# Kernel optimization log

Measured on AMD Instinct MI355X. Metric: run time of the kernel, lower is better.

The kernel has to match this reference:

```python
import jax, jax.numpy as jnp
import numpy as np

G = 8          # grid_size
DH = 32        # dim_head
EPS = 1e-5
INIT_LS = 1e-5


def setup_inputs() -> dict:
    key = jax.random.key(0)
    ks = jax.random.split(key, 8)
    B, H, W, C = 16, 128, 128, 256
    s = 1.0 / np.sqrt(C)
    return {
        "x": jax.random.normal(ks[0], (B, H, W, C), dtype=jnp.float32),
        "ln_w": jnp.ones((C,), jnp.float32),
        "ln_b": jnp.zeros((C,), jnp.float32),
        "in_proj_w": jax.random.uniform(ks[1], (3 * C, C), jnp.float32, -s, s),
        "in_proj_b": jnp.zeros((3 * C,), jnp.float32),
        "out_proj_w": jax.random.uniform(ks[2], (C, C), jnp.float32, -s, s),
        "out_proj_b": jnp.zeros((C,), jnp.float32),
        "gamma": jnp.full((C,), INIT_LS, jnp.float32),
    }


def _grid_attention(x, ln_w, ln_b, in_proj_w, in_proj_b, out_proj_w, out_proj_b, gamma):
    B, H, W, C = x.shape
    nh = C // DH
    # LayerNorm over channels
    mu = jnp.mean(x, axis=-1, keepdims=True)
    var = jnp.mean(jnp.square(x - mu), axis=-1, keepdims=True)
    x = (x - mu) * jax.lax.rsqrt(var + EPS) * ln_w + ln_b
    # grid partition: (B,G,H/G,G,W/G,C) -> (B,H/G,W/G,G,G,C) -> (N, G*G, C)
    hg, wg = H // G, W // G
    xw = x.reshape(B, G, hg, G, wg, C).transpose(0, 2, 4, 1, 3, 5)
    xw = xw.reshape(B * hg * wg, G * G, C)  # N windows of L=G*G tokens
    # MHSA (nn.MultiheadAttention semantics)
    qkv = xw @ in_proj_w.T + in_proj_b                      # (N, L, 3C)
    q, k, v = jnp.split(qkv, 3, axis=-1)
    N, L = xw.shape[0], xw.shape[1]
    q = q.reshape(N, L, nh, DH).transpose(0, 2, 1, 3)        # (N, nh, L, DH)
    k = k.reshape(N, L, nh, DH).transpose(0, 2, 1, 3)
    v = v.reshape(N, L, nh, DH).transpose(0, 2, 1, 3)
    scores = jnp.einsum("nhld,nhmd->nhlm", q, k) / np.sqrt(DH)
    attn = jax.nn.softmax(scores, axis=-1)
    out = jnp.einsum("nhlm,nhmd->nhld", attn, v)             # (N, nh, L, DH)
    out = out.transpose(0, 2, 1, 3).reshape(N, L, C)
    out = out @ out_proj_w.T + out_proj_b
    # LayerScale
    out = out * gamma
    # grid reverse: (B,H/G,W/G,G,G,C) -> (B,G,H/G,G,W/G,C) -> (B,H,W,C)
    out = out.reshape(B, hg, wg, G, G, C).transpose(0, 3, 1, 4, 2, 5)
    return out.reshape(B, H, W, C)


def reference(x, ln_w, ln_b, in_proj_w, in_proj_b, out_proj_w, out_proj_b, gamma):
    return _grid_attention(x, ln_w, ln_b, in_proj_w, in_proj_b,
                           out_proj_w, out_proj_b, gamma)
```

## Files before the change

### kernel.cpp

```cpp
#include <hip/hip_runtime.h>
#include <hip/hip_bf16.h>

typedef __attribute__((ext_vector_type(8))) short short8;
typedef __attribute__((ext_vector_type(4))) float f32x4;
typedef __attribute__((ext_vector_type(4))) unsigned short us4;
typedef __attribute__((ext_vector_type(2))) unsigned uint2v;

union U8 { unsigned u[4]; short8 s; };

__device__ __forceinline__ unsigned short f2b(float f) {
  unsigned u = __float_as_uint(f);
  u += 0x7FFFu + ((u >> 16) & 1u);
  return (unsigned short)(u >> 16);
}
__device__ __forceinline__ unsigned pkbf(float lo, float hi) {
  __hip_bfloat162 h = __float22bfloat162_rn(make_float2(lo, hi));
  unsigned u; __builtin_memcpy(&u, &h, 4);
  return u;
}
__device__ __forceinline__ void swp32(unsigned &a, unsigned &b) {
  uint2v r = __builtin_amdgcn_permlane32_swap(a, b, false, false);
  a = r.x; b = r.y;
}
__device__ __forceinline__ void swp16(unsigned &a, unsigned &b) {
  uint2v r = __builtin_amdgcn_permlane16_swap(a, b, false, false);
  a = r.x; b = r.y;
}
__device__ __forceinline__ float redq_sum(float v) {
  uint2v r = __builtin_amdgcn_permlane16_swap(__float_as_uint(v), __float_as_uint(v), false, false);
  v = __uint_as_float(r.x) + __uint_as_float(r.y);
  r = __builtin_amdgcn_permlane32_swap(__float_as_uint(v), __float_as_uint(v), false, false);
  return __uint_as_float(r.x) + __uint_as_float(r.y);
}
__device__ __forceinline__ float red5_sum(float v) {
  v += __shfl_xor(v, 8);
  return redq_sum(v);
}

__global__ __launch_bounds__(64) void prep(
    const float* __restrict__ wq, const float* __restrict__ wo,
    const float* __restrict__ gm, const float* __restrict__ bo,
    unsigned short* __restrict__ wbf, float* __restrict__ boG) {
  int d = blockIdx.x, lane = threadIdx.x;
  if (d < 768) {
    float4 wv = *(const float4*)(wq + (size_t)d * 256 + lane * 4);
    us4 o;
    o.x = f2b(wv.x); o.y = f2b(wv.y); o.z = f2b(wv.z); o.w = f2b(wv.w);
    *(us4*)(wbf + (size_t)d * 256 + lane * 4) = o;
  } else {
    int dd = d - 768;
    float g = gm[dd];
    float4 wv = *(const float4*)(wo + (size_t)dd * 256 + lane * 4);
    us4 o;
    o.x = f2b(wv.x * g); o.y = f2b(wv.y * g); o.z = f2b(wv.z * g); o.w = f2b(wv.w * g);
    *(us4*)(wbf + 196608 + (size_t)dd * 256 + lane * 4) = o;
    if (lane == 0) boG[dd] = bo[dd] * g;
  }
}

__global__ __launch_bounds__(512, 4) void grid_attn(
    const float* __restrict__ x,
    const float* __restrict__ lnw4,
    const float* __restrict__ lnb4,
    const unsigned short* __restrict__ Wqkv,
    const float* __restrict__ bqkv,
    const unsigned short* __restrict__ Wout,
    const float* __restrict__ boG,
    float* __restrict__ out) {

  __shared__ unsigned short ldsX[64 * 264];
  __shared__ unsigned short ldsY[64 * 264];
  __shared__ float ldsMu[64];
  __shared__ float ldsRs[64];

  const int tid = threadIdx.x;
  const int w   = tid >> 6;
  const int lid = tid & 63;
  const int l16 = lid & 15;
  const int lhi = lid >> 4;

  const int n  = blockIdx.x;
  const int b  = n >> 8;
  const int wi = (n >> 4) & 15;
  const int wj = n & 15;

  {
    float4 v[8];
    float2 p[8];
    #pragma unroll
    for (int t = 0; t < 8; ++t) {
      int l = w * 8 + t;
      int a = l >> 3, cg = l & 7;
      int hh = a * 16 + wi, ww = cg * 16 + wj;
      v[t] = *(const float4*)(x + ((size_t)((b * 128 + hh) * 128 + ww)) * 256 + lid * 4);
      p[t].x = v[t].x + v[t].y + v[t].z + v[t].w;
      p[t].y = v[t].x * v[t].x + v[t].y * v[t].y + v[t].z * v[t].z + v[t].w * v[t].w;
    }
    const int h1 = lid & 1, h2 = (lid >> 1) & 1, h4 = (lid >> 2) & 1;
    float2 q[4];
    #pragma unroll
    for (int i = 0; i < 4; ++i) {
      float sx = h1 ? p[i].x : p[i + 4].x, sy = h1 ? p[i].y : p[i + 4].y;
      float kx = h1 ? p[i + 4].x : p[i].x, ky = h1 ? p[i + 4].y : p[i].y;
      q[i].x = kx + __shfl_xor(sx, 1);
      q[i].y = ky + __shfl_xor(sy, 1);
    }
    float2 r2[2];
    #pragma unroll
    for (int i = 0; i < 2; ++i) {
      float sx = h2 ? q[i].x : q[i + 2].x, sy = h2 ? q[i].y : q[i + 2].y;
      float kx = h2 ? q[i + 2].x : q[i].x, ky = h2 ? q[i + 2].y : q[i].y;
      r2[i].x = kx + __shfl_xor(sx, 2);
      r2[i].y = ky + __shfl_xor(sy, 2);
    }
    float fx, fy;
    {
      float sx = h4 ? r2[0].x : r2[1].x, sy = h4 ? r2[0].y : r2[1].y;
      float kx = h4 ? r2[1].x : r2[0].x, ky = h4 ? r2[1].y : r2[0].y;
      fx = kx + __shfl_xor(sx, 4);
      fy = ky + __shfl_xor(sy, 4);
    }
    fx = red5_sum(fx);
    fy = red5_sum(fy);
    if (lid < 8) {
      int T = h1 * 4 + h2 * 2 + h4;
      float mu = fx * (1.0f / 256.0f);
      float var = fy * (1.0f / 256.0f) - mu * mu;
      ldsMu[w * 8 + T] = mu;
      ldsRs[w * 8 + T] = rsqrtf(var + 1e-5f);
    }
    float4 lw = *(const float4*)(lnw4 + lid * 4);
    float4 lb = *(const float4*)(lnb4 + lid * 4);
    #pragma unroll
    for (int t = 0; t < 8; ++t) {
      int l = w * 8 + t;
      float mu = ldsMu[w * 8 + t];
      float rs = ldsRs[w * 8 + t];
      float n0 = (v[t].x - mu) * rs * lw.x + lb.x;
      float n1 = (v[t].y - mu) * rs * lw.y + lb.y;
      float n2 = (v[t].z - mu) * rs * lw.z + lb.z;
      float n3 = (v[t].w - mu) * rs * lw.w + lb.w;
      uint2v o; o.x = pkbf(n0, n1); o.y = pkbf(n2, n3);
      *(uint2v*)(&ldsX[l * 264 + lid * 4]) = o;
    }
  }
  __syncthreads();

  short8 vtf[2][2];
  {
    float bv0 = bqkv[512 + w * 32 + l16];
    float bv1 = bqkv[512 + w * 32 + 16 + l16];
    f32x4 va[4][2];
    #pragma unroll
    for (int tt = 0; tt < 4; ++tt) {
      va[tt][0] = (f32x4){bv0, bv0, bv0, bv0};
      va[tt][1] = (f32x4){bv1, bv1, bv1, bv1};
    }
    const unsigned short* wvp = Wqkv + (size_t)(512 + w * 32 + l16) * 256 + lhi * 8;
    __builtin_amdgcn_s_setprio(1);
    #pragma unroll 4
    for (int kc = 0; kc < 8; ++kc) {
      short8 wv0 = *(const short8*)(wvp + kc * 32);
      short8 wv1 = *(const short8*)(wvp + 16 * 256 + kc * 32);
      #pragma unroll
      for (int tt = 0; tt < 4; ++tt) {
        short8 xf = *(const short8*)(&ldsX[(tt * 16 + l16) * 264 + kc * 32 + lhi * 8]);
        va[tt][0] = __builtin_amdgcn_mfma_f32_16x16x32_bf16(xf, wv0, va[tt][0], 0, 0, 0);
        va[tt][1] = __builtin_amdgcn_mfma_f32_16x16x32_bf16(xf, wv1, va[tt][1], 0, 0, 0);
      }
    }
    __builtin_amdgcn_s_setprio(0);
    #pragma unroll
    for (int dt = 0; dt < 2; ++dt) {
      unsigned bu[8];
      #pragma unroll
      for (int tt = 0; tt < 4; ++tt) {
        bu[tt * 2]     = pkbf(va[tt][dt][0], va[tt][dt][1]);
        bu[tt * 2 + 1] = pkbf(va[tt][dt][2], va[tt][dt][3]);
      }
      swp32(bu[0], bu[2]); swp32(bu[1], bu[3]); swp32(bu[4], bu[6]); swp32(bu[5], bu[7]);
      swp16(bu[0], bu[2]); swp16(bu[1], bu[3]); swp16(bu[4], bu[6]); swp16(bu[5], bu[7]);
      U8 z0, z1;
      z0.u[0] = bu[0]; z0.u[1] = bu[1]; z0.u[2] = bu[2]; z0.u[3] = bu[3];
      z1.u[0] = bu[4]; z1.u[1] = bu[5]; z1.u[2] = bu[6]; z1.u[3] = bu[7];
      vtf[dt][0] = z0.s;
      vtf[dt][1] = z1.s;
    }
  }

  short8 qf[4], kf[4];

  {
    f32x4 Cq0 = *(const f32x4*)(bqkv + w * 32 + lhi * 4);
    f32x4 Cq1 = *(const f32x4*)(bqkv + w * 32 + 16 + lhi * 4);
    f32x4 Ck0 = *(const f32x4*)(bqkv + 256 + w * 32 + lhi * 4);
    f32x4 Ck1 = *(const f32x4*)(bqkv + 256 + w * 32 + 16 + lhi * 4);
    f32x4 qa[2][4], ka[2][4];
    #pragma unroll
    for (int tt = 0; tt < 4; ++tt) {
      qa[0][tt] = Cq0; qa[1][tt] = Cq1;
      ka[0][tt] = Ck0; ka[1][tt] = Ck1;
    }
    const unsigned short* wqp = Wqkv + (size_t)(w * 32 + l16) * 256 + lhi * 8;
    const unsigned short* wkp = wqp + 256 * 256;
    __builtin_amdgcn_s_setprio(1);
    #pragma unroll 2
    for (int kc = 0; kc < 8; ++kc) {
      short8 wq0 = *(const short8*)(wqp + kc * 32);
      short8 wq1 = *(const short8*)(wqp + 16 * 256 + kc * 32);
      short8 wk0 = *(const short8*)(wkp + kc * 32);
      short8 wk1 = *(const short8*)(wkp + 16 * 256 + kc * 32);
      #pragma unroll
      for (int tt = 0; tt < 4; ++tt) {
        short8 xf = *(const short8*)(&ldsX[(tt * 16 + l16) * 264 + kc * 32 + lhi * 8]);
        qa[0][tt] = __builtin_amdgcn_mfma_f32_16x16x32_bf16(wq0, xf, qa[0][tt], 0, 0, 0);
        qa[1][tt] = __builtin_amdgcn_mfma_f32_16x16x32_bf16(wq1, xf, qa[1][tt], 0, 0, 0);
        ka[0][tt] = __builtin_amdgcn_mfma_f32_16x16x32_bf16(wk0, xf, ka[0][tt], 0, 0, 0);
        ka[1][tt] = __builtin_amdgcn_mfma_f32_16x16x32_bf16(wk1, xf, ka[1][tt], 0, 0, 0);
      }
    }
    __builtin_amdgcn_s_setprio(0);
    #pragma unroll
    for (int tt = 0; tt < 4; ++tt) {
      unsigned a0 = pkbf(qa[0][tt][0], qa[0][tt][1]), a1 = pkbf(qa[0][tt][2], qa[0][tt][3]);
      unsigned a2 = pkbf(qa[1][tt][0], qa[1][tt][1]), a3 = pkbf(qa[1][tt][2], qa[1][tt][3]);
      swp32(a0, a2); swp32(a1, a3);
      swp16(a0, a2); swp16(a1, a3);
      U8 z; z.u[0] = a0; z.u[1] = a1; z.u[2] = a2; z.u[3] = a3;
      qf[tt] = z.s;
      unsigned c0 = pkbf(ka[0][tt][0], ka[0][tt][1]), c1 = pkbf(ka[0][tt][2], ka[0][tt][3]);
      unsigned c2 = pkbf(ka[1][tt][0], ka[1][tt][1]), c3 = pkbf(ka[1][tt][2], ka[1][tt][3]);
      swp32(c0, c2); swp32(c1, c3);
      swp16(c0, c2); swp16(c1, c3);
      U8 y; y.u[0] = c0; y.u[1] = c1; y.u[2] = c2; y.u[3] = c3;
      kf[tt] = y.s;
    }
  }

  const float K2 = 0.25503487013594137f;
  #pragma unroll
  for (int nn = 0; nn < 4; ++nn) {
    f32x4 s[4];
    __builtin_amdgcn_s_setprio(1);
    #pragma unroll
    for (int m = 0; m < 4; ++m)
      s[m] = __builtin_amdgcn_mfma_f32_16x16x32_bf16(kf[m], qf[nn], (f32x4){0.f,0.f,0.f,0.f}, 0, 0, 0);
    __builtin_amdgcn_s_setprio(0);
    float sm[4];
    unsigned bu[8];
    #pragma unroll
    for (int m = 0; m < 4; ++m) {
      float e0 = exp2f(s[m][0] * K2);
      float e1 = exp2f(s[m][1] * K2);
      float e2 = exp2f(s[m][2] * K2);
      float e3 = exp2f(s[m][3] * K2);
      sm[m] = (e0 + e1) + (e2 + e3);
      bu[m * 2]     = pkbf(e0, e1);
      bu[m * 2 + 1] = pkbf(e2, e3);
    }
    float sum = (sm[0] + sm[1]) + (sm[2] + sm[3]);
    sum = redq_sum(sum);
    float iv = 1.0f / sum;
    swp32(bu[0], bu[2]); swp32(bu[1], bu[3]); swp32(bu[4], bu[6]); swp32(bu[5], bu[7]);
    swp16(bu[0], bu[2]); swp16(bu[1], bu[3]); swp16(bu[4], bu[6]); swp16(bu[5], bu[7]);
    U8 z0, z1;
    z0.u[0] = bu[0]; z0.u[1] = bu[1]; z0.u[2] = bu[2]; z0.u[3] = bu[3];
    z1.u[0] = bu[4]; z1.u[1] = bu[5]; z1.u[2] = bu[6]; z1.u[3] = bu[7];
    f32x4 ot0 = (f32x4){0.f,0.f,0.f,0.f};
    f32x4 ot1 = (f32x4){0.f,0.f,0.f,0.f};
    __builtin_amdgcn_s_setprio(1);
    ot0 = __builtin_amdgcn_mfma_f32_16x16x32_bf16(vtf[0][0], z0.s, ot0, 0, 0, 0);
    ot0 = __builtin_amdgcn_mfma_f32_16x16x32_bf16(vtf[0][1], z1.s, ot0, 0, 0, 0);
    ot1 = __builtin_amdgcn_mfma_f32_16x16x32_bf16(vtf[1][0], z0.s, ot1, 0, 0, 0);
    ot1 = __builtin_amdgcn_mfma_f32_16x16x32_bf16(vtf[1][1], z1.s, ot1, 0, 0, 0);
    __builtin_amdgcn_s_setprio(0);
    uint2v o0, o1;
    o0.x = pkbf(ot0[0] * iv, ot0[1] * iv);
    o0.y = pkbf(ot0[2] * iv, ot0[3] * iv);
    o1.x = pkbf(ot1[0] * iv, ot1[1] * iv);
    o1.y = pkbf(ot1[2] * iv, ot1[3] * iv);
    *(uint2v*)(&ldsY[(nn * 16 + l16) * 264 + w * 32 + lhi * 4]) = o0;
    *(uint2v*)(&ldsY[(nn * 16 + l16) * 264 + w * 32 + 16 + lhi * 4]) = o1;
  }

  __syncthreads();

  float ob0 = boG[w * 32 + l16];
  float ob1 = boG[w * 32 + 16 + l16];
  f32x4 ya[4][2];
  #pragma unroll
  for (int mt = 0; mt < 4; ++mt) {
    ya[mt][0] = (f32x4){ob0, ob0, ob0, ob0};
    ya[mt][1] = (f32x4){ob1, ob1, ob1, ob1};
  }
  {
    const unsigned short* wop = Wout + (size_t)(w * 32 + l16) * 256 + lhi * 8;
    __builtin_amdgcn_s_setprio(1);
    #pragma unroll 4
    for (int kc = 0; kc < 8; ++kc) {
      short8 wf0 = *(const short8*)(wop + kc * 32);
      short8 wf1 = *(const short8*)(wop + 16 * 256 + kc * 32);
      #pragma unroll
      for (int mt = 0; mt < 4; ++mt) {
        short8 af = *(const short8*)(&ldsY[(mt * 16 + l16) * 264 + kc * 32 + lhi * 8]);
        ya[mt][0] = __builtin_amdgcn_mfma_f32_16x16x32_bf16(af, wf0, ya[mt][0], 0, 0, 0);
        ya[mt][1] = __builtin_amdgcn_mfma_f32_16x16x32_bf16(af, wf1, ya[mt][1], 0, 0, 0);
      }
    }
    __builtin_amdgcn_s_setprio(0);
  }

  #pragma unroll
  for (int mt = 0; mt < 4; ++mt)
    #pragma unroll
    for (int r = 0; r < 4; ++r) {
      int row = mt * 16 + lhi * 4 + r;
      int a = row >> 3, cg = row & 7;
      int hh = a * 16 + wi, ww2 = cg * 16 + wj;
      float* pout = out + ((size_t)((b * 128 + hh) * 128 + ww2)) * 256 + w * 32;
      pout[l16]      = ya[mt][0][r];
      pout[l16 + 16] = ya[mt][1][r];
    }
}

extern "C" void kernel_launch(void* const* d_in, const int* in_sizes, int n_in,
                              void* d_out, int out_size, void* d_ws, size_t ws_size,
                              hipStream_t stream) {
  const float* x    = (const float*)d_in[0];
  const float* ln_w = (const float*)d_in[1];
  const float* ln_b = (const float*)d_in[2];
  const float* ipw  = (const float*)d_in[3];
  const float* ipb  = (const float*)d_in[4];
  const float* opw  = (const float*)d_in[5];
  const float* opb  = (const float*)d_in[6];
  const float* gm   = (const float*)d_in[7];

  unsigned short* wbf = (unsigned short*)d_ws;
  float* boG = (float*)(wbf + 262144);

  prep<<<1024, 64, 0, stream>>>(ipw, opw, gm, opb, wbf, boG);
  grid_attn<<<4096, 512, 0, stream>>>(x, ln_w, ln_b, wbf, ipb,
                                      wbf + 196608, boG, (float*)d_out);
}
```

Measured before the change: 320.7 us.

## Process two grid windows per block, reusing the LDS buffer for attention output

Each 512-thread block now handles two consecutive attention windows instead of one, so the grid is halved. Both windows' input rows are loaded at the start, putting more global reads in flight before LayerNorm. The separate ldsY buffer is dropped: the attention output is written back into that window's ldsX slot. This keeps LDS use the same while giving a double-buffered X. Compute for the two windows is interleaved across a few barriers. The cost is higher register pressure from holding two input tiles and two sets of Q/K/V fragments, which may reduce occupancy under the existing launch bounds.

```diff
diff --git a/kernel.cpp b/kernel.cpp
--- a/kernel.cpp
+++ b/kernel.cpp
@@ -68,10 +68,9 @@
     const float* __restrict__ boG,
     float* __restrict__ out) {
 
-  __shared__ unsigned short ldsX[64 * 264];
-  __shared__ unsigned short ldsY[64 * 264];
-  __shared__ float ldsMu[64];
-  __shared__ float ldsRs[64];
+  __shared__ unsigned short ldsX[2][64 * 264];
+  __shared__ float ldsMu[2][64];
+  __shared__ float ldsRs[2][64];
 
   const int tid = threadIdx.x;
   const int w   = tid >> 6;
@@ -79,75 +78,89 @@
   const int l16 = lid & 15;
   const int lhi = lid >> 4;
 
-  const int n  = blockIdx.x;
-  const int b  = n >> 8;
-  const int wi = (n >> 4) & 15;
-  const int wj = n & 15;
+  const int n0 = blockIdx.x * 2;
+
+  int bA = n0 >> 8,      wiA = (n0 >> 4) & 15,       wjA = n0 & 15;
+  int bB = (n0 + 1) >> 8, wiB = ((n0 + 1) >> 4) & 15, wjB = (n0 + 1) & 15;
 
   {
-    float4 v[8];
-    float2 p[8];
+    float4 vA[8], vB[8];
     #pragma unroll
     for (int t = 0; t < 8; ++t) {
       int l = w * 8 + t;
       int a = l >> 3, cg = l & 7;
-      int hh = a * 16 + wi, ww = cg * 16 + wj;
-      v[t] = *(const float4*)(x + ((size_t)((b * 128 + hh) * 128 + ww)) * 256 + lid * 4);
-      p[t].x = v[t].x + v[t].y + v[t].z + v[t].w;
-      p[t].y = v[t].x * v[t].x + v[t].y * v[t].y + v[t].z * v[t].z + v[t].w * v[t].w;
-    }
-    const int h1 = lid & 1, h2 = (lid >> 1) & 1, h4 = (lid >> 2) & 1;
-    float2 q[4];
-    #pragma unroll
-    for (int i = 0; i < 4; ++i) {
-      float sx = h1 ? p[i].x : p[i + 4].x, sy = h1 ? p[i].y : p[i + 4].y;
-      float kx = h1 ? p[i + 4].x : p[i].x, ky = h1 ? p[i + 4].y : p[i].y;
-      q[i].x = kx + __shfl_xor(sx, 1);
-      q[i].y = ky + __shfl_xor(sy, 1);
-    }
-    float2 r2[2];
-    #pragma unroll
-    for (int i = 0; i < 2; ++i) {
-      float sx = h2 ? q[i].x : q[i + 2].x, sy = h2 ? q[i].y : q[i + 2].y;
-      float kx = h2 ? q[i + 2].x : q[i].x, ky = h2 ? q[i + 2].y : q[i].y;
-      r2[i].x = kx + __shfl_xor(sx, 2);
-      r2[i].y = ky + __shfl_xor(sy, 2);
-    }
-    float fx, fy;
-    {
-      float sx = h4 ? r2[0].x : r2[1].x, sy = h4 ? r2[0].y : r2[1].y;
-      float kx = h4 ? r2[1].x : r2[0].x, ky = h4 ? r2[1].y : r2[0].y;
-      fx = kx + __shfl_xor(sx, 4);
-      fy = ky + __shfl_xor(sy, 4);
-    }
-    fx = red5_sum(fx);
-    fy = red5_sum(fy);
-    if (lid < 8) {
-      int T = h1 * 4 + h2 * 2 + h4;
-      float mu = fx * (1.0f / 256.0f);
-      float var = fy * (1.0f / 256.0f) - mu * mu;
-      ldsMu[w * 8 + T] = mu;
-      ldsRs[w * 8 + T] = rsqrtf(var + 1e-5f);
+      vA[t] = *(const float4*)(x + ((size_t)((bA * 128 + a * 16 + wiA) * 128 + cg * 16 + wjA)) * 256 + lid * 4);
+    }
+    #pragma unroll
+    for (int t = 0; t < 8; ++t) {
+      int l = w * 8 + t;
+      int a = l >> 3, cg = l & 7;
+      vB[t] = *(const float4*)(x + ((size_t)((bB * 128 + a * 16 + wiB) * 128 + cg * 16 + wjB)) * 256 + lid * 4);
     }
     float4 lw = *(const float4*)(lnw4 + lid * 4);
     float4 lb = *(const float4*)(lnb4 + lid * 4);
-    #pragma unroll
-    for (int t = 0; t < 8; ++t) {
-      int l = w * 8 + t;
-      float mu = ldsMu[w * 8 + t];
-      float rs = ldsRs[w * 8 + t];
-      float n0 = (v[t].x - mu) * rs * lw.x + lb.x;
-      float n1 = (v[t].y - mu) * rs * lw.y + lb.y;
-      float n2 = (v[t].z - mu) * rs * lw.z + lb.z;
-      float n3 = (v[t].w - mu) * rs * lw.w + lb.w;
-      uint2v o; o.x = pkbf(n0, n1); o.y = pkbf(n2, n3);
-      *(uint2v*)(&ldsX[l * 264 + lid * 4]) = o;
-    }
+    const int h1 = lid & 1, h2 = (lid >> 1) & 1, h4 = (lid >> 2) & 1;
+
+    auto stats_norm = [&](float4 (&v)[8], int vv) {
+      float2 p[8];
+      #pragma unroll
+      for (int t = 0; t < 8; ++t) {
+        p[t].x = v[t].x + v[t].y + v[t].z + v[t].w;
+        p[t].y = v[t].x * v[t].x + v[t].y * v[t].y + v[t].z * v[t].z + v[t].w * v[t].w;
+      }
+      float2 q[4];
+      #pragma unroll
+      for (int i = 0; i < 4; ++i) {
+        float sx = h1 ? p[i].x : p[i + 4].x, sy = h1 ? p[i].y : p[i + 4].y;
+        float kx = h1 ? p[i + 4].x : p[i].x, ky = h1 ? p[i + 4].y : p[i].y;
+        q[i].x = kx + __shfl_xor(sx, 1);
+        q[i].y = ky + __shfl_xor(sy, 1);
+      }
+      float2 r2[2];
+      #pragma unroll
+      for (int i = 0; i < 2; ++i) {
+        float sx = h2 ? q[i].x : q[i + 2].x, sy = h2 ? q[i].y : q[i + 2].y;
+        float kx = h2 ? q[i + 2].x : q[i].x, ky = h2 ? q[i + 2].y : q[i].y;
+        r2[i].x = kx + __shfl_xor(sx, 2);
+        r2[i].y = ky + __shfl_xor(sy, 2);
+      }
+      float fx, fy;
+      {
+        float sx = h4 ? r2[0].x : r2[1].x, sy = h4 ? r2[0].y : r2[1].y;
+        float kx = h4 ? r2[1].x : r2[0].x, ky = h4 ? r2[1].y : r2[0].y;
+        fx = kx + __shfl_xor(sx, 4);
+        fy = ky + __shfl_xor(sy, 4);
+      }
+      fx = red5_sum(fx);
+      fy = red5_sum(fy);
+      if (lid < 8) {
+        int T = h1 * 4 + h2 * 2 + h4;
+        float mu = fx * (1.0f / 256.0f);
+        float var = fy * (1.0f / 256.0f) - mu * mu;
+        ldsMu[vv][w * 8 + T] = mu;
+        ldsRs[vv][w * 8 + T] = rsqrtf(var + 1e-5f);
+      }
+      #pragma unroll
+      for (int t = 0; t < 8; ++t) {
+        int l = w * 8 + t;
+        float mu = ldsMu[vv][w * 8 + t];
+        float rs = ldsRs[vv][w * 8 + t];
+        float m0 = (v[t].x - mu) * rs * lw.x + lb.x;
+        float m1 = (v[t].y - mu) * rs * lw.y + lb.y;
+        float m2 = (v[t].z - mu) * rs * lw.z + lb.z;
+        float m3 = (v[t].w - mu) * rs * lw.w + lb.w;
+        uint2v o; o.x = pkbf(m0, m1); o.y = pkbf(m2, m3);
+        *(uint2v*)(&ldsX[vv][l * 264 + lid * 4]) = o;
+      }
+    };
+    stats_norm(vA, 0);
+    stats_norm(vB, 1);
   }
   __syncthreads();
 
-  short8 vtf[2][2];
-  {
+  const float K2 = 0.25503487013594137f;
+
+  auto Vg = [&](const unsigned short* xb, short8 (&vtf)[2][2]) {
     float bv0 = bqkv[512 + w * 32 + l16];
     float bv1 = bqkv[512 + w * 32 + 16 + l16];
     f32x4 va[4][2];
@@ -164,7 +177,7 @@
       short8 wv1 = *(const short8*)(wvp + 16 * 256 + kc * 32);
       #pragma unroll
       for (int tt = 0; tt < 4; ++tt) {
-        short8 xf = *(const short8*)(&ldsX[(tt * 16 + l16) * 264 + kc * 32 + lhi * 8]);
+        short8 xf = *(const short8*)(&xb[(tt * 16 + l16) * 264 + kc * 32 + lhi * 8]);
         va[tt][0] = __builtin_amdgcn_mfma_f32_16x16x32_bf16(xf, wv0, va[tt][0], 0, 0, 0);
         va[tt][1] = __builtin_amdgcn_mfma_f32_16x16x32_bf16(xf, wv1, va[tt][1], 0, 0, 0);
       }
@@ -186,11 +199,9 @@
       vtf[dt][0] = z0.s;
       vtf[dt][1] = z1.s;
     }
-  }
-
-  short8 qf[4], kf[4];
-
-  {
+  };
+
+  auto QKg = [&](const unsigned short* xb, short8 (&qf)[4], short8 (&kf)[4]) {
     f32x4 Cq0 = *(const f32x4*)(bqkv + w * 32 + lhi * 4);
     f32x4 Cq1 = *(const f32x4*)(bqkv + w * 32 + 16 + lhi * 4);
     f32x4 Ck0 = *(const f32x4*)(bqkv + 256 + w * 32 + lhi * 4);
@@ -212,7 +223,7 @@
       short8 wk1 = *(const short8*)(wkp + 16 * 256 + kc * 32);
       #pragma unroll
       for (int tt = 0; tt < 4; ++tt) {
-        short8 xf = *(const short8*)(&ldsX[(tt * 16 + l16) * 264 + kc * 32 + lhi * 8]);
+        short8 xf = *(const short8*)(&xb[(tt * 16 + l16) * 264 + kc * 32 + lhi * 8]);
         qa[0][tt] = __builtin_amdgcn_mfma_f32_16x16x32_bf16(wq0, xf, qa[0][tt], 0, 0, 0);
         qa[1][tt] = __builtin_amdgcn_mfma_f32_16x16x32_bf16(wq1, xf, qa[1][tt], 0, 0, 0);
         ka[0][tt] = __builtin_amdgcn_mfma_f32_16x16x32_bf16(wk0, xf, ka[0][tt], 0, 0, 0);
@@ -235,65 +246,64 @@
       U8 y; y.u[0] = c0; y.u[1] = c1; y.u[2] = c2; y.u[3] = c3;
       kf[tt] = y.s;
     }
-  }
-
-  const float K2 = 0.25503487013594137f;
-  #pragma unroll
-  for (int nn = 0; nn < 4; ++nn) {
-    f32x4 s[4];
-    __builtin_amdgcn_s_setprio(1);
-    #pragma unroll
-    for (int m = 0; m < 4; ++m)
-      s[m] = __builtin_amdgcn_mfma_f32_16x16x32_bf16(kf[m], qf[nn], (f32x4){0.f,0.f,0.f,0.f}, 0, 0, 0);
-    __builtin_amdgcn_s_setprio(0);
-    float sm[4];
-    unsigned bu[8];
-    #pragma unroll
-    for (int m = 0; m < 4; ++m) {
-      float e0 = exp2f(s[m][0] * K2);
-      float e1 = exp2f(s[m][1] * K2);
-      float e2 = exp2f(s[m][2] * K2);
-      float e3 = exp2f(s[m][3] * K2);
-      sm[m] = (e0 + e1) + (e2 + e3);
-      bu[m * 2]     = pkbf(e0, e1);
-      bu[m * 2 + 1] = pkbf(e2, e3);
-    }
-    float sum = (sm[0] + sm[1]) + (sm[2] + sm[3]);
-    sum = redq_sum(sum);
-    float iv = 1.0f / sum;
-    swp32(bu[0], bu[2]); swp32(bu[1], bu[3]); swp32(bu[4], bu[6]); swp32(bu[5], bu[7]);
-    swp16(bu[0], bu[2]); swp16(bu[1], bu[3]); swp16(bu[4], bu[6]); swp16(bu[5], bu[7]);
-    U8 z0, z1;
-    z0.u[0] = bu[0]; z0.u[1] = bu[1]; z0.u[2] = bu[2]; z0.u[3] = bu[3];
-    z1.u[0] = bu[4]; z1.u[1] = bu[5]; z1.u[2] = bu[6]; z1.u[3] = bu[7];
-    f32x4 ot0 = (f32x4){0.f,0.f,0.f,0.f};
-    f32x4 ot1 = (f32x4){0.f,0.f,0.f,0.f};
-    __builtin_amdgcn_s_setprio(1);
-    ot0 = __builtin_amdgcn_mfma_f32_16x16x32_bf16(vtf[0][0], z0.s, ot0, 0, 0, 0);
-    ot0 = __builtin_amdgcn_mfma_f32_16x16x32_bf16(vtf[0][1], z1.s, ot0, 0, 0, 0);
-    ot1 = __builtin_amdgcn_mfma_f32_16x16x32_bf16(vtf[1][0], z0.s, ot1, 0, 0, 0);
-    ot1 = __builtin_amdgcn_mfma_f32_16x16x32_bf16(vtf[1][1], z1.s, ot1, 0, 0, 0);
-    __builtin_amdgcn_s_setprio(0);
-    uint2v o0, o1;
-    o0.x = pkbf(ot0[0] * iv, ot0[1] * iv);
-    o0.y = pkbf(ot0[2] * iv, ot0[3] * iv);
-    o1.x = pkbf(ot1[0] * iv, ot1[1] * iv);
-    o1.y = pkbf(ot1[2] * iv, ot1[3] * iv);
-    *(uint2v*)(&ldsY[(nn * 16 + l16) * 264 + w * 32 + lhi * 4]) = o0;
-    *(uint2v*)(&ldsY[(nn * 16 + l16) * 264 + w * 32 + 16 + lhi * 4]) = o1;
-  }
-
-  __syncthreads();
-
-  float ob0 = boG[w * 32 + l16];
-  float ob1 = boG[w * 32 + 16 + l16];
-  f32x4 ya[4][2];
-  #pragma unroll
-  for (int mt = 0; mt < 4; ++mt) {
-    ya[mt][0] = (f32x4){ob0, ob0, ob0, ob0};
-    ya[mt][1] = (f32x4){ob1, ob1, ob1, ob1};
-  }
-  {
+  };
+
+  auto SCg = [&](unsigned short* xb, short8 (&vtf)[2][2], short8 (&qf)[4], short8 (&kf)[4]) {
+    #pragma unroll
+    for (int nn = 0; nn < 4; ++nn) {
+      f32x4 s[4];
+      __builtin_amdgcn_s_setprio(1);
+      #pragma unroll
+      for (int m = 0; m < 4; ++m)
+        s[m] = __builtin_amdgcn_mfma_f32_16x16x32_bf16(kf[m], qf[nn], (f32x4){0.f,0.f,0.f,0.f}, 0, 0, 0);
+      __builtin_amdgcn_s_setprio(0);
+      float sm[4];
+      unsigned bu[8];
+      #pragma unroll
+      for (int m = 0; m < 4; ++m) {
+        float e0 = exp2f(s[m][0] * K2);
+        float e1 = exp2f(s[m][1] * K2);
+        float e2 = exp2f(s[m][2] * K2);
+        float e3 = exp2f(s[m][3] * K2);
+        sm[m] = (e0 + e1) + (e2 + e3);
+        bu[m * 2]     = pkbf(e0, e1);
+        bu[m * 2 + 1] = pkbf(e2, e3);
+      }
+      float sum = (sm[0] + sm[1]) + (sm[2] + sm[3]);
+      sum = redq_sum(sum);
+      float iv = 1.0f / sum;
+      swp32(bu[0], bu[2]); swp32(bu[1], bu[3]); swp32(bu[4], bu[6]); swp32(bu[5], bu[7]);
+      swp16(bu[0], bu[2]); swp16(bu[1], bu[3]); swp16(bu[4], bu[6]); swp16(bu[5], bu[7]);
+      U8 z0, z1;
+      z0.u[0] = bu[0]; z0.u[1] = bu[1]; z0.u[2] = bu[2]; z0.u[3] = bu[3];
+      z1.u[0] = bu[4]; z1.u[1] = bu[5]; z1.u[2] = bu[6]; z1.u[3] = bu[7];
+      f32x4 ot0 = (f32x4){0.f,0.f,0.f,0.f};
+      f32x4 ot1 = (f32x4){0.f,0.f,0.f,0.f};
+      __builtin_amdgcn_s_setprio(1);
+      ot0 = __builtin_amdgcn_mfma_f32_16x16x32_bf16(vtf[0][0], z0.s, ot0, 0, 0, 0);
+      ot0 = __builtin_amdgcn_mfma_f32_16x16x32_bf16(vtf[0][1], z1.s, ot0, 0, 0, 0);
+      ot1 = __builtin_amdgcn_mfma_f32_16x16x32_bf16(vtf[1][0], z0.s, ot1, 0, 0, 0);
+      ot1 = __builtin_amdgcn_mfma_f32_16x16x32_bf16(vtf[1][1], z1.s, ot1, 0, 0, 0);
+      __builtin_amdgcn_s_setprio(0);
+      uint2v o0, o1;
+      o0.x = pkbf(ot0[0] * iv, ot0[1] * iv);
+      o0.y = pkbf(ot0[2] * iv, ot0[3] * iv);
+      o1.x = pkbf(ot1[0] * iv, ot1[1] * iv);
+      o1.y = pkbf(ot1[2] * iv, ot1[3] * iv);
+      *(uint2v*)(&xb[(nn * 16 + l16) * 264 + w * 32 + lhi * 4]) = o0;
+      *(uint2v*)(&xb[(nn * 16 + l16) * 264 + w * 32 + 16 + lhi * 4]) = o1;
+    }
+  };
+
+  auto OPg = [&](const unsigned short* xb, int b, int wi, int wj) {
+    float ob0 = boG[w * 32 + l16];
+    float ob1 = boG[w * 32 + 16 + l16];
+    f32x4 ya[4][2];
+    #pragma unroll
+    for (int mt = 0; mt < 4; ++mt) {
+      ya[mt][0] = (f32x4){ob0, ob0, ob0, ob0};
+      ya[mt][1] = (f32x4){ob1, ob1, ob1, ob1};
+    }
     const unsigned short* wop = Wout + (size_t)(w * 32 + l16) * 256 + lhi * 8;
     __builtin_amdgcn_s_setprio(1);
     #pragma unroll 4
@@ -302,25 +312,40 @@
       short8 wf1 = *(const short8*)(wop + 16 * 256 + kc * 32);
       #pragma unroll
       for (int mt = 0; mt < 4; ++mt) {
-        short8 af = *(const short8*)(&ldsY[(mt * 16 + l16) * 264 + kc * 32 + lhi * 8]);
+        short8 af = *(const short8*)(&xb[(mt * 16 + l16) * 264 + kc * 32 + lhi * 8]);
         ya[mt][0] = __builtin_amdgcn_mfma_f32_16x16x32_bf16(af, wf0, ya[mt][0], 0, 0, 0);
         ya[mt][1] = __builtin_amdgcn_mfma_f32_16x16x32_bf16(af, wf1, ya[mt][1], 0, 0, 0);
       }
     }
     __builtin_amdgcn_s_setprio(0);
-  }
-
-  #pragma unroll
-  for (int mt = 0; mt < 4; ++mt)
-    #pragma unroll
-    for (int r = 0; r < 4; ++r) {
-      int row = mt * 16 + lhi * 4 + r;
-      int a = row >> 3, cg = row & 7;
-      int hh = a * 16 + wi, ww2 = cg * 16 + wj;
-      float* pout = out + ((size_t)((b * 128 + hh) * 128 + ww2)) * 256 + w * 32;
-      pout[l16]      = ya[mt][0][r];
-      pout[l16 + 16] = ya[mt][1][r];
-    }
+    #pragma unroll
+    for (int mt = 0; mt < 4; ++mt)
+      #pragma unroll
+      for (int r = 0; r < 4; ++r) {
+        int row = mt * 16 + lhi * 4 + r;
+        int a = row >> 3, cg = row & 7;
+        float* pout = out + ((size_t)((b * 128 + a * 16 + wi) * 128 + cg * 16 + wj)) * 256 + w * 32;
+        pout[l16]      = ya[mt][0][r];
+        pout[l16 + 16] = ya[mt][1][r];
+      }
+  };
+
+  short8 vtfA[2][2], qfA[4], kfA[4];
+  Vg(&ldsX[0][0], vtfA);
+  QKg(&ldsX[0][0], qfA, kfA);
+  __syncthreads();
+
+  SCg(&ldsX[0][0], vtfA, qfA, kfA);
+
+  short8 vtfB[2][2], qfB[4], kfB[4];
+  Vg(&ldsX[1][0], vtfB);
+  QKg(&ldsX[1][0], qfB, kfB);
+  __syncthreads();
+
+  SCg(&ldsX[1][0], vtfB, qfB, kfB);
+  OPg(&ldsX[0][0], bA, wiA, wjA);
+  __syncthreads();
+  OPg(&ldsX[1][0], bB, wiB, wjB);
 }
 
 extern "C" void kernel_launch(void* const* d_in, const int* in_sizes, int n_in,
@@ -339,6 +364,6 @@
   float* boG = (float*)(wbf + 262144);
 
   prep<<<1024, 64, 0, stream>>>(ipw, opw, gm, opb, wbf, boG);
-  grid_attn<<<4096, 512, 0, stream>>>(x, ln_w, ln_b, wbf, ipb,
+  grid_attn<<<2048, 512, 0, stream>>>(x, ln_w, ln_b, wbf, ipb,
                                       wbf + 196608, boG, (float*)d_out);
 }
```

New measurement: 314.1 us, median of 2. 1.02x faster.
